# Kernel tuning notes

Measured on AMD Instinct MI355X. Metric: run time of the kernel, lower is better.

The kernel has to match this reference:

```python
import jax, jax.numpy as jnp
import numpy as np

DIM, QK, PDIM = 256, 16, 64
EPS = 1e-5  # BatchNorm2d / GroupNorm default eps
SCALE = QK ** -0.5


def bn_eval(y, w, b, rm, rv):
    # eval-mode BatchNorm2d folded to per-channel scale+shift
    inv = w / jnp.sqrt(rv + EPS)
    return y * inv[None, :, None, None] + (b - rm * inv)[None, :, None, None]


def setup_inputs() -> dict:
    key = jax.random.key(0)
    ks = jax.random.split(key, 14)
    qkv_out = 2 * QK + PDIM  # 96
    d = {}
    d["x"] = jax.random.normal(ks[0], (4, DIM, 64, 64), jnp.float32)
    # GroupNorm(1, pdim) affine params
    d["gn_w"] = 1.0 + 0.1 * jax.random.normal(ks[1], (PDIM,), jnp.float32)
    d["gn_b"] = 0.1 * jax.random.normal(ks[2], (PDIM,), jnp.float32)
    # qkv Conv2d_BN: 1x1 conv (no bias) + BN
    d["qkv_w"] = 0.05 * jax.random.normal(ks[3], (qkv_out, PDIM), jnp.float32)
    d["qkv_bn_w"] = 1.0 + 0.1 * jax.random.normal(ks[4], (qkv_out,), jnp.float32)
    d["qkv_bn_b"] = 0.1 * jax.random.normal(ks[5], (qkv_out,), jnp.float32)
    d["qkv_rm"] = 0.1 * jax.random.normal(ks[6], (qkv_out,), jnp.float32)
    d["qkv_rv"] = jax.random.uniform(ks[7], (qkv_out,), jnp.float32, 0.5, 1.5)
    # proj Conv2d_BN: 1x1 conv (no bias) + BN (bn_weight_init=0 in torch; use random for nontrivial output)
    d["proj_w"] = 0.05 * jax.random.normal(ks[8], (DIM, DIM), jnp.float32)
    d["proj_bn_w"] = 1.0 + 0.1 * jax.random.normal(ks[9], (DIM,), jnp.float32)
    d["proj_bn_b"] = 0.1 * jax.random.normal(ks[10], (DIM,), jnp.float32)
    d["proj_rm"] = 0.1 * jax.random.normal(ks[11], (DIM,), jnp.float32)
    d["proj_rv"] = jax.random.uniform(ks[12], (DIM,), jnp.float32, 0.5, 1.5)
    return d


def reference(x, gn_w, gn_b, qkv_w, qkv_bn_w, qkv_bn_b, qkv_rm, qkv_rv,
              proj_w, proj_bn_w, proj_bn_b, proj_rm, proj_rv):
    B, C, H, W = x.shape
    N = H * W
    x1, x2 = x[:, :PDIM], x[:, PDIM:]
    # GroupNorm with 1 group: normalize over (C, H, W) per sample
    mu = jnp.mean(x1, axis=(1, 2, 3), keepdims=True)
    var = jnp.var(x1, axis=(1, 2, 3), keepdims=True)
    x1n = (x1 - mu) * jax.lax.rsqrt(var + EPS)
    x1n = x1n * gn_w[None, :, None, None] + gn_b[None, :, None, None]
    # 1x1 conv + BN (eval)
    qkv = bn_eval(jnp.einsum('bchw,oc->bohw', x1n, qkv_w),
                  qkv_bn_w, qkv_bn_b, qkv_rm, qkv_rv)
    q = qkv[:, :QK].reshape(B, QK, N)
    k = qkv[:, QK:2 * QK].reshape(B, QK, N)
    v = qkv[:, 2 * QK:].reshape(B, PDIM, N)
    # attn[b, n, m] = sum_c q[b,c,n] * k[b,c,m]
    attn = jnp.einsum('bcn,bcm->bnm', q, k) * SCALE
    attn = jax.nn.softmax(attn, axis=-1)
    # x1 = v @ attn^T : out[b,p,n] = sum_m v[b,p,m] * attn[b,n,m]
    x1o = jnp.einsum('bpm,bnm->bpn', v, attn).reshape(B, PDIM, H, W)
    y = jnp.concatenate([x1o, x2], axis=1)
    y = jax.nn.silu(y)
    y = bn_eval(jnp.einsum('bchw,oc->bohw', y, proj_w),
                proj_bn_w, proj_bn_b, proj_rm, proj_rv)
    return y
```

## Files before the change

### kernel.cpp

```cpp
#include <hip/hip_runtime.h>
#include <hip/hip_bf16.h>
#include <math.h>

static constexpr int B_ = 4;
static constexpr int C_ = 256;
static constexpr int PD_ = 64;
static constexpr int N_ = 4096;
static constexpr int O96_ = 96;
static constexpr float EPS_ = 1e-5f;
static constexpr float SCALE_ = 0.25f;
static constexpr float LOG2E_ = 1.4426950408889634f;

typedef __attribute__((ext_vector_type(8))) short short8v;
typedef __attribute__((ext_vector_type(4))) float f32x4;

__device__ inline short f2bf(float x) {
    __hip_bfloat16 h = __float2bfloat16(x);
    short r; __builtin_memcpy(&r, &h, 2); return r;
}
__device__ inline float bf2f(short s) {
    union { float f; unsigned u; } v; v.u = ((unsigned)(unsigned short)s) << 16;
    return v.f;
}
__device__ inline unsigned pack_bf2(float lo, float hi) {
    return ((unsigned)(unsigned short)f2bf(hi) << 16) | (unsigned)(unsigned short)f2bf(lo);
}
__device__ inline float silu_(float v) { return v / (1.0f + __expf(-v)); }
__device__ inline float exp2_fast(float x) {
#if __has_builtin(__builtin_amdgcn_exp2f)
    return __builtin_amdgcn_exp2f(x);
#else
    return __expf(x * 0.6931471805599453f);
#endif
}

__global__ __launch_bounds__(256) void k_gnw(const float* __restrict__ x,
        float* __restrict__ part,
        const float* __restrict__ pw,  const float* __restrict__ bnw,
        const float* __restrict__ bnb, const float* __restrict__ rm,
        const float* __restrict__ rv,  short* __restrict__ wbf,
        float* __restrict__ beta) {
    if (blockIdx.x >= 256) {
        const int idx = (blockIdx.x - 256) * 256 + threadIdx.x;
        const int o = idx >> 8, c = idx & 255;
        const float inv = bnw[o] * rsqrtf(rv[o] + EPS_);
        wbf[idx] = f2bf(pw[idx] * inv);
        if (c == 0) beta[o] = bnb[o] - rm[o] * inv;
        return;
    }
    const int blk = blockIdx.x;
    const int b = blk >> 6, c = blk & 63;
    const float* p = x + (size_t)(b * C_ + c) * N_;
    float s = 0.f, q = 0.f;
    for (int i = threadIdx.x; i < N_; i += 256) {
        float v = p[i]; s += v; q += v * v;
    }
    for (int d = 1; d < 64; d <<= 1) {
        s += __shfl_xor(s, d, 64);
        q += __shfl_xor(q, d, 64);
    }
    __shared__ float ls[4], lq[4];
    const int lane = threadIdx.x & 63, wid = threadIdx.x >> 6;
    if (lane == 0) { ls[wid] = s; lq[wid] = q; }
    __syncthreads();
    if (threadIdx.x == 0) {
        part[2 * blk]     = ls[0] + ls[1] + ls[2] + ls[3];
        part[2 * blk + 1] = lq[0] + lq[1] + lq[2] + lq[3];
    }
}

__global__ __launch_bounds__(64) void k_gn_fin(const float* __restrict__ part,
                                               float* __restrict__ stats) {
    const int b = blockIdx.x;
    float s = part[2 * (b * 64 + threadIdx.x)];
    float q = part[2 * (b * 64 + threadIdx.x) + 1];
    for (int d = 1; d < 64; d <<= 1) {
        s += __shfl_xor(s, d, 64);
        q += __shfl_xor(q, d, 64);
    }
    if (threadIdx.x == 0) {
        const float inv_n = 1.0f / (float)(PD_ * N_);
        float mu = s * inv_n;
        float var = q * inv_n - mu * mu;
        stats[2 * b]     = mu;
        stats[2 * b + 1] = rsqrtf(var + EPS_);
    }
}

__global__ __launch_bounds__(512) void k_qkv(const float* __restrict__ x,
        const float* __restrict__ gnw, const float* __restrict__ gnb,
        const float* __restrict__ qw,  const float* __restrict__ bnw,
        const float* __restrict__ bnb, const float* __restrict__ rm,
        const float* __restrict__ rv,  const float* __restrict__ stats,
        short* __restrict__ qT, short* __restrict__ kfrag, short* __restrict__ vfrag) {
    __shared__ float wl[O96_ * PD_];
    __shared__ float binv[O96_], bbeta[O96_];
    const int t = threadIdx.x;
    const int b = blockIdx.x >> 6;
    const int n0 = (blockIdx.x & 63) << 6;
    for (int i = t; i < O96_ * PD_; i += 512) wl[i] = qw[i];
    for (int o = t; o < O96_; o += 512) {
        float inv  = bnw[o] * rsqrtf(rv[o] + EPS_);
        float beta = bnb[o] - rm[o] * inv;
        if (o < 16) { inv *= SCALE_ * LOG2E_; beta *= SCALE_ * LOG2E_; }
        binv[o] = inv; bbeta[o] = beta;
    }
    const float mu = stats[2 * b], rs = stats[2 * b + 1];
    __syncthreads();
    const int nl = t & 63;
    const int n  = n0 + nl;
    const int og = t >> 6;
    float xn[PD_];
    const float* xb = x + (size_t)b * C_ * N_ + n;
    #pragma unroll
    for (int c = 0; c < PD_; ++c)
        xn[c] = (xb[(size_t)c * N_] - mu) * rs * gnw[c] + gnb[c];
    const size_t mblk = (size_t)b * 64 + (n >> 6);
    short* qrow = qT + ((size_t)b * N_ + n) * 16;
    short* kbase = kfrag + mblk * 1024;
    short* vbase = vfrag + mblk * 4096;
    const int mt = nl >> 4, colm = nl & 15;
    const int ks = nl >> 5, gv = (nl >> 3) & 3, jv = nl & 7;
    for (int o = og * 12; o < og * 12 + 12; ++o) {
        const float4* wr = (const float4*)&wl[o * PD_];
        float a = 0.f;
        #pragma unroll
        for (int c4 = 0; c4 < 16; ++c4) {
            float4 w4 = wr[c4];
            a += w4.x * xn[4*c4] + w4.y * xn[4*c4+1] + w4.z * xn[4*c4+2] + w4.w * xn[4*c4+3];
        }
        short val = f2bf(a * binv[o] + bbeta[o]);
        if (o < 16) {
            qrow[o] = val;
        } else if (o < 32) {
            const int c = o - 16;
            kbase[((mt * 2 + (c >> 3)) * 16 + colm) * 8 + (c & 7)] = val;
        } else {
            const int p = o - 32;
            vbase[(((ks * 4 + (p >> 4)) * 64) + gv * 16 + (p & 15)) * 8 + jv] = val;
        }
    }
}

__global__ __launch_bounds__(256) void k_attn(const short* __restrict__ qT,
        const short* __restrict__ kfrag, const short* __restrict__ vfrag,
        short* __restrict__ apart) {
    __shared__ __align__(16) short Pl_all[4][2][2][1024];

    const int wg  = blockIdx.x;
    const int swz = (wg & 7) * 128 + (wg >> 3);
    const int b   = swz >> 8;
    const int mq  = (swz >> 5) & 7;
    const int nt  = swz & 31;
    const int n0  = nt << 7;

    const int t    = threadIdx.x;
    const int w    = t >> 6;
    const int lane = t & 63;
    const int g    = lane >> 4;
    const int col  = lane & 15;
    const int c7   = col & 7;

    const short* qbase = qT + ((size_t)b * N_ + n0 + w * 32 + col) * 16;
    const short* kfb = kfrag + ((size_t)b * 64 + mq * 8) * 1024;
    const short* vfb = vfrag + ((size_t)b * 64 + mq * 8) * 4096;

    short8v a_q0 = 0, a_q1 = 0;
    if (g < 2) {
        a_q0 = *(const short8v*)(qbase + 8 * g);
        a_q1 = *(const short8v*)(qbase + 256 + 8 * g);
    }
    short8v onesf = 0;
    if (col == 0) {
        #pragma unroll
        for (int j = 0; j < 8; ++j) onesf[j] = (short)0x3F80;
    }

    f32x4 acc0[5], acc1[5];
    #pragma unroll
    for (int pt = 0; pt < 5; ++pt) { acc0[pt] = 0.f; acc1[pt] = 0.f; }

    for (int it = 0; it < 8; ++it) {
        const short* kit = kfb + it * 1024;
        const short* vit = vfb + it * 4096;
        short* Pl0 = &Pl_all[w][it & 1][0][0];
        short* Pl1 = &Pl_all[w][it & 1][1][0];
        short8v kr[4];
        #pragma unroll
        for (int mt = 0; mt < 4; ++mt) {
            kr[mt] = 0;
            if (g < 2) kr[mt] = *(const short8v*)(kit + ((mt * 2 + g) * 16 + col) * 8);
        }
        short8v vpre[8];
        #pragma unroll
        for (int j = 0; j < 8; ++j)
            vpre[j] = *(const short8v*)(vit + (j * 64 + g * 16 + col) * 8);
        f32x4 s[4];
        #pragma unroll
        for (int mt = 0; mt < 4; ++mt) {
            f32x4 z = 0.f;
            s[mt] = __builtin_amdgcn_mfma_f32_16x16x32_bf16(kr[mt], a_q0, z, 0, 0, 0);
        }
        #pragma unroll
        for (int mt = 0; mt < 4; ++mt) {
            unsigned lo = pack_bf2(exp2_fast(s[mt][0]), exp2_fast(s[mt][1]));
            unsigned hi = pack_bf2(exp2_fast(s[mt][2]), exp2_fast(s[mt][3]));
            const int slot = (2 * mt + (g >> 1)) ^ c7;
            *(uint2*)(Pl0 + col * 64 + slot * 8 + 4 * (g & 1)) = make_uint2(lo, hi);
        }
        #pragma unroll
        for (int mt = 0; mt < 4; ++mt) {
            f32x4 z = 0.f;
            s[mt] = __builtin_amdgcn_mfma_f32_16x16x32_bf16(kr[mt], a_q1, z, 0, 0, 0);
        }
        #pragma unroll
        for (int mt = 0; mt < 4; ++mt) {
            unsigned lo = pack_bf2(exp2_fast(s[mt][0]), exp2_fast(s[mt][1]));
            unsigned hi = pack_bf2(exp2_fast(s[mt][2]), exp2_fast(s[mt][3]));
            const int slot = (2 * mt + (g >> 1)) ^ c7;
            *(uint2*)(Pl1 + col * 64 + slot * 8 + 4 * (g & 1)) = make_uint2(lo, hi);
        }
        asm volatile("s_waitcnt lgkmcnt(0)" ::: "memory");
        __builtin_amdgcn_sched_barrier(0);
        #pragma unroll
        for (int ks = 0; ks < 2; ++ks) {
            short8v pa0 = *(const short8v*)(Pl0 + col * 64 + (((4 * ks + g) ^ c7) << 3));
            short8v pa1 = *(const short8v*)(Pl1 + col * 64 + (((4 * ks + g) ^ c7) << 3));
            acc0[4] = __builtin_amdgcn_mfma_f32_16x16x32_bf16(pa0, onesf, acc0[4], 0, 0, 0);
            acc1[4] = __builtin_amdgcn_mfma_f32_16x16x32_bf16(pa1, onesf, acc1[4], 0, 0, 0);
            #pragma unroll
            for (int pt = 0; pt < 4; ++pt) {
                acc0[pt] = __builtin_amdgcn_mfma_f32_16x16x32_bf16(pa0, vpre[ks * 4 + pt], acc0[pt], 0, 0, 0);
                acc1[pt] = __builtin_amdgcn_mfma_f32_16x16x32_bf16(pa1, vpre[ks * 4 + pt], acc1[pt], 0, 0, 0);
            }
        }
    }
    short* po = apart + (size_t)((b * 8 + mq) * 32 + nt) * 8448;
    #pragma unroll
    for (int pt = 0; pt < 4; ++pt) {
        #pragma unroll
        for (int r = 0; r < 4; ++r) {
            po[(w * 32 + 4 * g + r) * 64 + pt * 16 + col]      = f2bf(acc0[pt][r]);
            po[(w * 32 + 16 + 4 * g + r) * 64 + pt * 16 + col] = f2bf(acc1[pt][r]);
        }
    }
    if (col == 0) {
        float* ms = (float*)(po + 8192);
        #pragma unroll
        for (int r = 0; r < 4; ++r) {
            ms[w * 32 + 4 * g + r]      = acc0[4][r];
            ms[w * 32 + 16 + 4 * g + r] = acc1[4][r];
        }
    }
}

__global__ __launch_bounds__(256) void k_proj2(const short* __restrict__ apart,
        const float* __restrict__ x, const short* __restrict__ wbf,
        const float* __restrict__ beta, float* __restrict__ out) {
    __shared__ __align__(16) short ybf[32 * 256];
    const int t  = threadIdx.x;
    const int nt = blockIdx.x;
    const int b  = blockIdx.y;
    const int n0 = nt << 5;

    {
        const int nn = t >> 3, pg = t & 7;
        const int qloc = ((nt & 3) << 5) + nn;
        const short* pbase = apart + (size_t)((b * 8) * 32 + (nt >> 2)) * 8448;
        float oacc[8] = {0.f, 0.f, 0.f, 0.f, 0.f, 0.f, 0.f, 0.f};
        float Ssum = 0.f;
        #pragma unroll
        for (int k = 0; k < 8; ++k) {
            const short* pk = pbase + (size_t)k * 32 * 8448;
            Ssum += ((const float*)(pk + 8192))[qloc];
            short8v a = *(const short8v*)(pk + qloc * 64 + pg * 8);
            #pragma unroll
            for (int j = 0; j < 8; ++j) oacc[j] += bf2f(a[j]);
        }
        const float inv = 1.0f / Ssum;
        const int slot = pg ^ (nn & 7);
        *(uint4*)(ybf + nn * 256 + slot * 8) = make_uint4(
            pack_bf2(silu_(oacc[0] * inv), silu_(oacc[1] * inv)),
            pack_bf2(silu_(oacc[2] * inv), silu_(oacc[3] * inv)),
            pack_bf2(silu_(oacc[4] * inv), silu_(oacc[5] * inv)),
            pack_bf2(silu_(oacc[6] * inv), silu_(oacc[7] * inv)));
    }
    {
        const int nn = t & 31, cg = t >> 5;
        #pragma unroll
        for (int s3 = 0; s3 < 3; ++s3) {
            const int cb = 64 + cg * 24 + s3 * 8;
            unsigned pk4[4];
            #pragma unroll
            for (int j = 0; j < 4; ++j) {
                float v0 = x[((size_t)(b * C_ + cb + 2 * j)) * N_ + n0 + nn];
                float v1 = x[((size_t)(b * C_ + cb + 2 * j + 1)) * N_ + n0 + nn];
                pk4[j] = pack_bf2(silu_(v0), silu_(v1));
            }
            const int slot = (8 + cg * 3 + s3) ^ (nn & 7);
            *(uint4*)(ybf + nn * 256 + slot * 8) = make_uint4(pk4[0], pk4[1], pk4[2], pk4[3]);
        }
    }
    __syncthreads();
    const int w = t >> 6, lane = t & 63;
    const int col = lane & 15, g = lane >> 4;
    const int o_base = w << 6;
    f32x4 acc[4][2];
    #pragma unroll
    for (int ot = 0; ot < 4; ++ot) { acc[ot][0] = 0.f; acc[ot][1] = 0.f; }
    #pragma unroll
    for (int kk = 0; kk < 8; ++kk) {
        short8v bf0 = *(const short8v*)(ybf + col * 256 + (((kk * 4 + g) ^ (col & 7)) << 3));
        short8v bf1 = *(const short8v*)(ybf + (16 + col) * 256 + (((kk * 4 + g) ^ (col & 7)) << 3));
        #pragma unroll
        for (int ot = 0; ot < 4; ++ot) {
            short8v af = *(const short8v*)(wbf + (size_t)(o_base + ot * 16 + col) * C_ + kk * 32 + g * 8);
            acc[ot][0] = __builtin_amdgcn_mfma_f32_16x16x32_bf16(af, bf0, acc[ot][0], 0, 0, 0);
            acc[ot][1] = __builtin_amdgcn_mfma_f32_16x16x32_bf16(af, bf1, acc[ot][1], 0, 0, 0);
        }
    }
    #pragma unroll
    for (int ot = 0; ot < 4; ++ot) {
        #pragma unroll
        for (int r = 0; r < 4; ++r) {
            const int o = o_base + ot * 16 + 4 * g + r;
            const float be = beta[o];
            float* po = out + ((size_t)(b * C_ + o)) * N_ + n0 + col;
            po[0]  = acc[ot][0][r] + be;
            po[16] = acc[ot][1][r] + be;
        }
    }
}

extern "C" void kernel_launch(void* const* d_in, const int* in_sizes, int n_in,
                              void* d_out, int out_size, void* d_ws, size_t ws_size,
                              hipStream_t stream) {
    const float* x   = (const float*)d_in[0];
    const float* gnw = (const float*)d_in[1];
    const float* gnb = (const float*)d_in[2];
    const float* qw  = (const float*)d_in[3];
    const float* qbw = (const float*)d_in[4];
    const float* qbb = (const float*)d_in[5];
    const float* qrm = (const float*)d_in[6];
    const float* qrv = (const float*)d_in[7];
    const float* pw  = (const float*)d_in[8];
    const float* pbw = (const float*)d_in[9];
    const float* pbb = (const float*)d_in[10];
    const float* prm = (const float*)d_in[11];
    const float* prv = (const float*)d_in[12];
    float* out = (float*)d_out;
    char* wsb = (char*)d_ws;

    float* part  = (float*)wsb;
    float* stats = (float*)(wsb + 2048);
    short* wbf   = (short*)(wsb + 4096);
    float* beta  = (float*)(wsb + 135168);
    short* qTb   = (short*)(wsb + 139264);
    short* kfrag = (short*)(wsb + 663552);
    short* vfrag = (short*)(wsb + 1187840);
    short* apart = (short*)(wsb + 3284992);

    k_gnw<<<512, 256, 0, stream>>>(x, part, pw, pbw, pbb, prm, prv, wbf, beta);
    k_gn_fin<<<4, 64, 0, stream>>>(part, stats);
    k_qkv<<<256, 512, 0, stream>>>(x, gnw, gnb, qw, qbw, qbb, qrm, qrv, stats, qTb, kfrag, vfrag);
    k_attn<<<1024, 256, 0, stream>>>(qTb, kfrag, vfrag, apart);
    k_proj2<<<dim3(128, 4), 256, 0, stream>>>(apart, x, wbf, beta, out);
}
```

Baseline: 68.66 us.

## Permute K fragment layout so exp'd scores feed PV MFMA from registers

The K fragment layout written by the QKV kernel is permuted so that the S=K·Q MFMA output lanes directly match the A-operand layout needed by the P·V MFMA. This removes the LDS round-trip (store, waitcnt, reload) for the softmax probabilities in the attention kernel, along with the LDS allocation. It couples the two kernels' layouts tightly and relies on the permutation being correct across the MFMA register layouts.

```diff
diff --git a/kernel.cpp b/kernel.cpp
--- a/kernel.cpp
+++ b/kernel.cpp
@@ -119,7 +119,8 @@
     short* qrow = qT + ((size_t)b * N_ + n) * 16;
     short* kbase = kfrag + mblk * 1024;
     short* vbase = vfrag + mblk * 4096;
-    const int mt = nl >> 4, colm = nl & 15;
+    const int mtk  = 2 * ((nl >> 2) & 1) + (nl >> 5);
+    const int colk = 4 * ((nl >> 3) & 3) + (nl & 3);
     const int ks = nl >> 5, gv = (nl >> 3) & 3, jv = nl & 7;
     for (int o = og * 12; o < og * 12 + 12; ++o) {
         const float4* wr = (const float4*)&wl[o * PD_];
@@ -134,7 +135,7 @@
             qrow[o] = val;
         } else if (o < 32) {
             const int c = o - 16;
-            kbase[((mt * 2 + (c >> 3)) * 16 + colm) * 8 + (c & 7)] = val;
+            kbase[((mtk * 2 + (c >> 3)) * 16 + colk) * 8 + (c & 7)] = val;
         } else {
             const int p = o - 32;
             vbase[(((ks * 4 + (p >> 4)) * 64) + gv * 16 + (p & 15)) * 8 + jv] = val;
@@ -145,8 +146,6 @@
 __global__ __launch_bounds__(256) void k_attn(const short* __restrict__ qT,
         const short* __restrict__ kfrag, const short* __restrict__ vfrag,
         short* __restrict__ apart) {
-    __shared__ __align__(16) short Pl_all[4][2][2][1024];
-
     const int wg  = blockIdx.x;
     const int swz = (wg & 7) * 128 + (wg >> 3);
     const int b   = swz >> 8;
@@ -159,7 +158,6 @@
     const int lane = t & 63;
     const int g    = lane >> 4;
     const int col  = lane & 15;
-    const int c7   = col & 7;
 
     const short* qbase = qT + ((size_t)b * N_ + n0 + w * 32 + col) * 16;
     const short* kfb = kfrag + ((size_t)b * 64 + mq * 8) * 1024;
@@ -183,8 +181,6 @@
     for (int it = 0; it < 8; ++it) {
         const short* kit = kfb + it * 1024;
         const short* vit = vfb + it * 4096;
-        short* Pl0 = &Pl_all[w][it & 1][0][0];
-        short* Pl1 = &Pl_all[w][it & 1][1][0];
         short8v kr[4];
         #pragma unroll
         for (int mt = 0; mt < 4; ++mt) {
@@ -201,38 +197,38 @@
             f32x4 z = 0.f;
             s[mt] = __builtin_amdgcn_mfma_f32_16x16x32_bf16(kr[mt], a_q0, z, 0, 0, 0);
         }
-        #pragma unroll
-        for (int mt = 0; mt < 4; ++mt) {
-            unsigned lo = pack_bf2(exp2_fast(s[mt][0]), exp2_fast(s[mt][1]));
-            unsigned hi = pack_bf2(exp2_fast(s[mt][2]), exp2_fast(s[mt][3]));
-            const int slot = (2 * mt + (g >> 1)) ^ c7;
-            *(uint2*)(Pl0 + col * 64 + slot * 8 + 4 * (g & 1)) = make_uint2(lo, hi);
-        }
+        union { unsigned u[4]; short8v v; } p0k0, p0k1, p1k0, p1k1;
+        p0k0.u[0] = pack_bf2(exp2_fast(s[0][0]), exp2_fast(s[0][1]));
+        p0k0.u[1] = pack_bf2(exp2_fast(s[0][2]), exp2_fast(s[0][3]));
+        p0k0.u[2] = pack_bf2(exp2_fast(s[2][0]), exp2_fast(s[2][1]));
+        p0k0.u[3] = pack_bf2(exp2_fast(s[2][2]), exp2_fast(s[2][3]));
+        p0k1.u[0] = pack_bf2(exp2_fast(s[1][0]), exp2_fast(s[1][1]));
+        p0k1.u[1] = pack_bf2(exp2_fast(s[1][2]), exp2_fast(s[1][3]));
+        p0k1.u[2] = pack_bf2(exp2_fast(s[3][0]), exp2_fast(s[3][1]));
+        p0k1.u[3] = pack_bf2(exp2_fast(s[3][2]), exp2_fast(s[3][3]));
         #pragma unroll
         for (int mt = 0; mt < 4; ++mt) {
             f32x4 z = 0.f;
             s[mt] = __builtin_amdgcn_mfma_f32_16x16x32_bf16(kr[mt], a_q1, z, 0, 0, 0);
         }
-        #pragma unroll
-        for (int mt = 0; mt < 4; ++mt) {
-            unsigned lo = pack_bf2(exp2_fast(s[mt][0]), exp2_fast(s[mt][1]));
-            unsigned hi = pack_bf2(exp2_fast(s[mt][2]), exp2_fast(s[mt][3]));
-            const int slot = (2 * mt + (g >> 1)) ^ c7;
-            *(uint2*)(Pl1 + col * 64 + slot * 8 + 4 * (g & 1)) = make_uint2(lo, hi);
-        }
-        asm volatile("s_waitcnt lgkmcnt(0)" ::: "memory");
-        __builtin_amdgcn_sched_barrier(0);
-        #pragma unroll
-        for (int ks = 0; ks < 2; ++ks) {
-            short8v pa0 = *(const short8v*)(Pl0 + col * 64 + (((4 * ks + g) ^ c7) << 3));
-            short8v pa1 = *(const short8v*)(Pl1 + col * 64 + (((4 * ks + g) ^ c7) << 3));
-            acc0[4] = __builtin_amdgcn_mfma_f32_16x16x32_bf16(pa0, onesf, acc0[4], 0, 0, 0);
-            acc1[4] = __builtin_amdgcn_mfma_f32_16x16x32_bf16(pa1, onesf, acc1[4], 0, 0, 0);
-            #pragma unroll
-            for (int pt = 0; pt < 4; ++pt) {
-                acc0[pt] = __builtin_amdgcn_mfma_f32_16x16x32_bf16(pa0, vpre[ks * 4 + pt], acc0[pt], 0, 0, 0);
-                acc1[pt] = __builtin_amdgcn_mfma_f32_16x16x32_bf16(pa1, vpre[ks * 4 + pt], acc1[pt], 0, 0, 0);
-            }
+        p1k0.u[0] = pack_bf2(exp2_fast(s[0][0]), exp2_fast(s[0][1]));
+        p1k0.u[1] = pack_bf2(exp2_fast(s[0][2]), exp2_fast(s[0][3]));
+        p1k0.u[2] = pack_bf2(exp2_fast(s[2][0]), exp2_fast(s[2][1]));
+        p1k0.u[3] = pack_bf2(exp2_fast(s[2][2]), exp2_fast(s[2][3]));
+        p1k1.u[0] = pack_bf2(exp2_fast(s[1][0]), exp2_fast(s[1][1]));
+        p1k1.u[1] = pack_bf2(exp2_fast(s[1][2]), exp2_fast(s[1][3]));
+        p1k1.u[2] = pack_bf2(exp2_fast(s[3][0]), exp2_fast(s[3][1]));
+        p1k1.u[3] = pack_bf2(exp2_fast(s[3][2]), exp2_fast(s[3][3]));
+        acc0[4] = __builtin_amdgcn_mfma_f32_16x16x32_bf16(p0k0.v, onesf, acc0[4], 0, 0, 0);
+        acc0[4] = __builtin_amdgcn_mfma_f32_16x16x32_bf16(p0k1.v, onesf, acc0[4], 0, 0, 0);
+        acc1[4] = __builtin_amdgcn_mfma_f32_16x16x32_bf16(p1k0.v, onesf, acc1[4], 0, 0, 0);
+        acc1[4] = __builtin_amdgcn_mfma_f32_16x16x32_bf16(p1k1.v, onesf, acc1[4], 0, 0, 0);
+        #pragma unroll
+        for (int pt = 0; pt < 4; ++pt) {
+            acc0[pt] = __builtin_amdgcn_mfma_f32_16x16x32_bf16(p0k0.v, vpre[pt],     acc0[pt], 0, 0, 0);
+            acc0[pt] = __builtin_amdgcn_mfma_f32_16x16x32_bf16(p0k1.v, vpre[4 + pt], acc0[pt], 0, 0, 0);
+            acc1[pt] = __builtin_amdgcn_mfma_f32_16x16x32_bf16(p1k0.v, vpre[pt],     acc1[pt], 0, 0, 0);
+            acc1[pt] = __builtin_amdgcn_mfma_f32_16x16x32_bf16(p1k1.v, vpre[4 + pt], acc1[pt], 0, 0, 0);
         }
     }
     short* po = apart + (size_t)((b * 8 + mq) * 32 + nt) * 8448;
```

Result: no change. 68.03 us (-0.9%).
